# Kernel optimization log

Measured on AMD Instinct MI355X. Metric: run time of the kernel, lower is better.

Reference implementation:

```python
import jax, jax.numpy as jnp
import numpy as np

OBS_DIM = 32
HIDDEN = 64


def setup_inputs() -> dict:
    key = jax.random.key(0)
    k1, k2, k3, k4 = jax.random.split(key, 4)
    # PyTorch-style uniform init bound 1/sqrt(hidden)
    bnd = 1.0 / np.sqrt(HIDDEN)
    y = jax.random.normal(k1, (256, 2048, OBS_DIM), dtype=jnp.float32)
    Wx = jax.random.uniform(k2, (OBS_DIM, 4 * HIDDEN), minval=-bnd, maxval=bnd, dtype=jnp.float32)
    Wh = jax.random.uniform(k3, (HIDDEN, 4 * HIDDEN), minval=-bnd, maxval=bnd, dtype=jnp.float32)
    b = jax.random.uniform(k4, (4 * HIDDEN,), minval=-bnd, maxval=bnd, dtype=jnp.float32)
    return {"y": y, "Wx": Wx, "Wh": Wh, "b": b}


def reference(y, Wx, Wh, b):
    # y: [B, T, obs_dim] -> LSTM features [B, T, hidden]
    B, T, _ = y.shape
    H = Wh.shape[0]
    yT = jnp.swapaxes(y, 0, 1)  # [T, B, D]

    def step(carry, x_t):
        h, c = carry
        gates = x_t @ Wx + h @ Wh + b  # [B, 4H]
        i, f, g, o = jnp.split(gates, 4, axis=-1)  # PyTorch gate order i,f,g,o
        i = jax.nn.sigmoid(i)
        f = jax.nn.sigmoid(f)
        g = jnp.tanh(g)
        o = jax.nn.sigmoid(o)
        c_new = f * c + i * g
        h_new = o * jnp.tanh(c_new)
        return (h_new, c_new), h_new

    h0 = jnp.zeros((B, H), dtype=y.dtype)
    c0 = jnp.zeros((B, H), dtype=y.dtype)
    _, hs = jax.lax.scan(step, (h0, c0), yT)  # hs: [T, B, H]
    return jnp.swapaxes(hs, 0, 1)  # [B, T, H]
```

## Files before the change

### kernel.cpp

```cpp
#include <hip/hip_runtime.h>

#define BB 256
#define TT 2048
#define DD 32
#define HH 64
#define GG 256
#define OB 8

__device__ __forceinline__ float fast_sig(float x) {
    return __builtin_amdgcn_rcpf(1.0f + __expf(-x));
}
__device__ __forceinline__ float rdlane(float v, int k) {
    return __uint_as_float(__builtin_amdgcn_readlane(__float_as_uint(v), k));
}
__device__ __forceinline__ void lds_barrier() {
    asm volatile("s_waitcnt lgkmcnt(0)" ::: "memory");
    __builtin_amdgcn_s_barrier();
    asm volatile("" ::: "memory");
}

__global__ __launch_bounds__(256, 1) void lstm_ksplit_kernel(
    const float* __restrict__ y,
    const float* __restrict__ Wx,
    const float* __restrict__ Wh,
    const float* __restrict__ b,
    float* __restrict__ out)
{
    const int j = threadIdx.x;
    const int w = j >> 6;
    const int l = j & 63;
    const int batch = blockIdx.x;
    const int kb = 16 * w;

    __shared__ float4 gbuf[2][4][HH];
    __shared__ float obuf[2][OB][HH];

    float wh[4][16];
#pragma unroll
    for (int g = 0; g < 4; ++g)
#pragma unroll
        for (int k = 0; k < 16; ++k)
            wh[g][k] = Wh[(kb + k) * GG + g * HH + l];
    float wx[4][8];
#pragma unroll
    for (int g = 0; g < 4; ++g)
#pragma unroll
        for (int d = 0; d < 8; ++d)
            wx[g][d] = Wx[(8 * w + d) * GG + g * HH + l];
    float bj[4];
#pragma unroll
    for (int g = 0; g < 4; ++g) bj[g] = (w == 0) ? b[g * HH + l] : 0.0f;

    float c = 0.0f, h = 0.0f;

    const float* ybase = y + (size_t)batch * (TT * DD) + 8 * w;
    float* obase = out + (size_t)batch * (TT * HH);

    float4 xa[2], xb[2];
    float a0[4], a1[4];
    {
        const float4* r0 = (const float4*)ybase;
        float4 x00 = r0[0], x01 = r0[1];
        const float* xf = (const float*)&x00;
        const float* xg = (const float*)&x01;
#pragma unroll
        for (int g = 0; g < 4; ++g) { a0[g] = bj[g]; a1[g] = 0.0f; }
#pragma unroll
        for (int d = 0; d < 4; ++d)
#pragma unroll
            for (int g = 0; g < 4; ++g) a0[g] = fmaf(xf[d], wx[g][d], a0[g]);
#pragma unroll
        for (int d = 0; d < 4; ++d)
#pragma unroll
            for (int g = 0; g < 4; ++g) a1[g] = fmaf(xg[d], wx[g][d + 4], a1[g]);
        const float4* r1 = (const float4*)(ybase + DD);
        xa[0] = r1[0]; xa[1] = r1[1];
    }
    __syncthreads();

#define STEP(XC, XN, BUFI, TI, TL)                                            \
    {                                                                         \
                   \
        _Pragma("unroll")                                                     \
        for (int k = 0; k < 8; ++k) {                                         \
            const float hk = rdlane(h, kb + k);                               \
            _Pragma("unroll")                                                 \
            for (int g = 0; g < 4; ++g) a0[g] = fmaf(hk, wh[g][k], a0[g]);    \
        }                                                                     \
        _Pragma("unroll")                                                     \
        for (int k = 8; k < 16; ++k) {                                        \
            const float hk = rdlane(h, kb + k);                               \
            _Pragma("unroll")                                                 \
            for (int g = 0; g < 4; ++g) a1[g] = fmaf(hk, wh[g][k], a1[g]);    \
        }                                                                     \
            \
        float4 pw;                                                            \
        pw.x = a0[0] + a1[0]; pw.y = a0[1] + a1[1];                           \
        pw.z = a0[2] + a1[2]; pw.w = a0[3] + a1[3];                           \
        gbuf[BUFI][w][l] = pw;                                                \
                \
        {                                                                     \
            const float* xf_ = (const float*)&XC[0];                          \
            _Pragma("unroll")                                                 \
            for (int g = 0; g < 4; ++g) a0[g] = bj[g];                        \
            _Pragma("unroll")                                                 \
            for (int d = 0; d < 4; ++d)                                       \
                _Pragma("unroll")                                             \
                for (int g = 0; g < 4; ++g)                                   \
                    a0[g] = fmaf(xf_[d], wx[g][d], a0[g]);                    \
        }                                                                     \
        {                                                                     \
            const int tn_ = ((TI) + 2 < TT) ? ((TI) + 2) : (TT - 1);          \
            const float4* nr_ = (const float4*)(ybase + (size_t)tn_ * DD);    \
            XN[0] = nr_[0]; XN[1] = nr_[1];                                   \
        }                                                                     \
        lds_barrier();                                                        \
                  \
        const float4 P0 = gbuf[BUFI][0][l];                                   \
        const float4 P1 = gbuf[BUFI][1][l];                                   \
        const float4 P2 = gbuf[BUFI][2][l];                                   \
        const float4 P3 = gbuf[BUFI][3][l];                                   \
        {                                                                     \
            const float* xg_ = (const float*)&XC[1];                          \
            _Pragma("unroll")                                                 \
            for (int g = 0; g < 4; ++g) a1[g] = 0.0f;                         \
            _Pragma("unroll")                                                 \
            for (int d = 0; d < 4; ++d)                                       \
                _Pragma("unroll")                                             \
                for (int g = 0; g < 4; ++g)                                   \
                    a1[g] = fmaf(xg_[d], wx[g][d + 4], a1[g]);                \
        }                                                                     \
                   \
        const float gi_ = (P0.x + P1.x) + (P2.x + P3.x);                      \
        const float gf_ = (P0.y + P1.y) + (P2.y + P3.y);                      \
        const float gg_ = (P0.z + P1.z) + (P2.z + P3.z);                      \
        const float go_ = (P0.w + P1.w) + (P2.w + P3.w);                      \
        const float i_ = fast_sig(gi_);                                       \
        const float f_ = fast_sig(gf_);                                       \
        const float g_ = fmaf(2.0f, fast_sig(2.0f * gg_), -1.0f);             \
        const float o_ = fast_sig(go_);                                       \
        c = fmaf(f_, c, i_ * g_);                                             \
        h = o_ * fmaf(2.0f, fast_sig(2.0f * c), -1.0f);        \
        if (w == 0) obuf[obi][TL][l] = h;                                     \
    }

    for (int t0 = 0; t0 < TT; t0 += OB) {
        const int obi = (t0 >> 3) & 1;
#pragma unroll
        for (int tp = 0; tp < OB; tp += 2) {
            STEP(xa, xb, 0, t0 + tp, tp)
            STEP(xb, xa, 1, t0 + tp + 1, tp + 1)
        }
        lds_barrier();
        {
            const int r = j >> 5;
            const int ci = (j & 31) * 2;
            const float2 v = *(const float2*)&obuf[obi][r][ci];
            *(float2*)&obase[(size_t)(t0 + r) * HH + ci] = v;
        }
    }
#undef STEP
}

extern "C" void kernel_launch(void* const* d_in, const int* in_sizes, int n_in,
                              void* d_out, int out_size, void* d_ws, size_t ws_size,
                              hipStream_t stream) {
    const float* y  = (const float*)d_in[0];
    const float* Wx = (const float*)d_in[1];
    const float* Wh = (const float*)d_in[2];
    const float* b  = (const float*)d_in[3];
    float* out = (float*)d_out;

    lstm_ksplit_kernel<<<BB, GG, 0, stream>>>(y, Wx, Wh, b, out);
}
```

Before: 961.2 us.

## Process two batch elements per block and fold log2e into weights

Each 512-thread block now runs two independent LSTM recurrences, one per group of four waves, halving the grid to 128 blocks. Weights and bias are pre-scaled by log2e so the sigmoid/tanh use exp2 directly, removing a multiply per activation. The goal is to interleave two latency-bound chains on one CU. The cost is that half the CUs sit idle and barriers now span eight waves.

Measured after the change: 1.349 ms. +40.3%, slower.

```diff
diff --git a/kernel.cpp b/kernel.cpp
--- a/kernel.cpp
+++ b/kernel.cpp
@@ -6,9 +6,16 @@
 #define HH 64
 #define GG 256
 #define OB 8
+#define LOG2E 1.44269504088896f
 
-__device__ __forceinline__ float fast_sig(float x) {
-    return __builtin_amdgcn_rcpf(1.0f + __expf(-x));
+#if __has_builtin(__builtin_amdgcn_exp2f)
+#define EXP2F(x) __builtin_amdgcn_exp2f(x)
+#else
+#define EXP2F(x) exp2f(x)
+#endif
+
+__device__ __forceinline__ float sig_e2(float y) {
+    return __builtin_amdgcn_rcpf(1.0f + EXP2F(-y));
 }
 __device__ __forceinline__ float rdlane(float v, int k) {
     return __uint_as_float(__builtin_amdgcn_readlane(__float_as_uint(v), k));
@@ -19,42 +26,44 @@
     asm volatile("" ::: "memory");
 }
 
-__global__ __launch_bounds__(256, 1) void lstm_ksplit_kernel(
+__global__ __launch_bounds__(512, 1) void lstm_pair_kernel(
     const float* __restrict__ y,
     const float* __restrict__ Wx,
     const float* __restrict__ Wh,
     const float* __restrict__ b,
     float* __restrict__ out)
 {
-    const int j = threadIdx.x;
-    const int w = j >> 6;
-    const int l = j & 63;
-    const int batch = blockIdx.x;
-    const int kb = 16 * w;
+    const int tid = threadIdx.x;
+    const int wv  = tid >> 6;
+    const int eh  = wv >> 2;
+    const int w   = wv & 3;
+    const int l   = tid & 63;
+    const int elem = blockIdx.x * 2 + eh;
+    const int kb  = 16 * w;
 
-    __shared__ float4 gbuf[2][4][HH];
-    __shared__ float obuf[2][OB][HH];
+    __shared__ float4 gbuf[2][2][4][HH];
+    __shared__ float  obuf[2][2][OB][HH];
 
     float wh[4][16];
 #pragma unroll
     for (int g = 0; g < 4; ++g)
 #pragma unroll
         for (int k = 0; k < 16; ++k)
-            wh[g][k] = Wh[(kb + k) * GG + g * HH + l];
+            wh[g][k] = Wh[(kb + k) * GG + g * HH + l] * LOG2E;
     float wx[4][8];
 #pragma unroll
     for (int g = 0; g < 4; ++g)
 #pragma unroll
         for (int d = 0; d < 8; ++d)
-            wx[g][d] = Wx[(8 * w + d) * GG + g * HH + l];
+            wx[g][d] = Wx[(8 * w + d) * GG + g * HH + l] * LOG2E;
     float bj[4];
 #pragma unroll
-    for (int g = 0; g < 4; ++g) bj[g] = (w == 0) ? b[g * HH + l] : 0.0f;
+    for (int g = 0; g < 4; ++g) bj[g] = (w == 0) ? b[g * HH + l] * LOG2E : 0.0f;
 
     float c = 0.0f, h = 0.0f;
 
-    const float* ybase = y + (size_t)batch * (TT * DD) + 8 * w;
-    float* obase = out + (size_t)batch * (TT * HH);
+    const float* ybase = y + (size_t)elem * (TT * DD) + 8 * w;
+    float* obase = out + (size_t)elem * (TT * HH);
 
     float4 xa[2], xb[2];
     float a0[4], a1[4];
@@ -93,12 +102,12 @@
             _Pragma("unroll")                                                 \
             for (int g = 0; g < 4; ++g) a1[g] = fmaf(hk, wh[g][k], a1[g]);    \
         }                                                                     \
-            \
+                                \
         float4 pw;                                                            \
         pw.x = a0[0] + a1[0]; pw.y = a0[1] + a1[1];                           \
         pw.z = a0[2] + a1[2]; pw.w = a0[3] + a1[3];                           \
-        gbuf[BUFI][w][l] = pw;                                                \
-                \
+        gbuf[BUFI][eh][w][l] = pw;                                            \
+        \
         {                                                                     \
             const float* xf_ = (const float*)&XC[0];                          \
             _Pragma("unroll")                                                 \
@@ -116,10 +125,10 @@
         }                                                                     \
         lds_barrier();                                                        \
                   \
-        const float4 P0 = gbuf[BUFI][0][l];                                   \
-        const float4 P1 = gbuf[BUFI][1][l];                                   \
-        const float4 P2 = gbuf[BUFI][2][l];                                   \
-        const float4 P3 = gbuf[BUFI][3][l];                                   \
+        const float4 P0 = gbuf[BUFI][eh][0][l];                               \
+        const float4 P1 = gbuf[BUFI][eh][1][l];                               \
+        const float4 P2 = gbuf[BUFI][eh][2][l];                               \
+        const float4 P3 = gbuf[BUFI][eh][3][l];                               \
         {                                                                     \
             const float* xg_ = (const float*)&XC[1];                          \
             _Pragma("unroll")                                                 \
@@ -130,18 +139,20 @@
                 for (int g = 0; g < 4; ++g)                                   \
                     a1[g] = fmaf(xg_[d], wx[g][d + 4], a1[g]);                \
         }                                                                     \
-                   \
+         \
         const float gi_ = (P0.x + P1.x) + (P2.x + P3.x);                      \
         const float gf_ = (P0.y + P1.y) + (P2.y + P3.y);                      \
         const float gg_ = (P0.z + P1.z) + (P2.z + P3.z);                      \
         const float go_ = (P0.w + P1.w) + (P2.w + P3.w);                      \
-        const float i_ = fast_sig(gi_);                                       \
-        const float f_ = fast_sig(gf_);                                       \
-        const float g_ = fmaf(2.0f, fast_sig(2.0f * gg_), -1.0f);             \
-        const float o_ = fast_sig(go_);                                       \
+        const float i_ = sig_e2(gi_);                                         \
+        const float f_ = sig_e2(gf_);                                         \
+        const float g_ = fmaf(2.0f, sig_e2(2.0f * gg_), -1.0f);     \
+        const float o_ = sig_e2(go_);                                         \
         c = fmaf(f_, c, i_ * g_);                                             \
-        h = o_ * fmaf(2.0f, fast_sig(2.0f * c), -1.0f);        \
-        if (w == 0) obuf[obi][TL][l] = h;                                     \
+                                   \
+        h = o_ * fmaf(2.0f, __builtin_amdgcn_rcpf(                            \
+                1.0f + EXP2F(c * (-2.0f * LOG2E))), -1.0f);                   \
+        if (w == 0) obuf[obi][eh][TL][l] = h;                                 \
     }
 
     for (int t0 = 0; t0 < TT; t0 += OB) {
@@ -153,10 +164,13 @@
         }
         lds_barrier();
         {
-            const int r = j >> 5;
-            const int ci = (j & 31) * 2;
-            const float2 v = *(const float2*)&obuf[obi][r][ci];
-            *(float2*)&obase[(size_t)(t0 + r) * HH + ci] = v;
+            const int jj = tid & 255;
+            const int e2 = tid >> 8;
+            const int r  = jj >> 5;
+            const int ci = (jj & 31) * 2;
+            float* ob2 = out + (size_t)(blockIdx.x * 2 + e2) * (TT * HH);
+            const float2 v = *(const float2*)&obuf[obi][e2][r][ci];
+            *(float2*)&ob2[(size_t)(t0 + r) * HH + ci] = v;
         }
     }
 #undef STEP
@@ -171,5 +185,5 @@
     const float* b  = (const float*)d_in[3];
     float* out = (float*)d_out;
 
-    lstm_ksplit_kernel<<<BB, GG, 0, stream>>>(y, Wx, Wh, b, out);
+    lstm_pair_kernel<<<BB / 2, 512, 0, stream>>>(y, Wx, Wh, b, out);
 }
```
